# Kernel optimization log

Measured on AMD Instinct MI355X. Metric: run time of the kernel, lower is better.

Reference implementation:

```python
import jax, jax.numpy as jnp
import numpy as np

B, T, D, F0, F1 = 128, 256, 512, 2048, 1024
EPS = 1e-5  # BatchNorm1d eps


def _bn_relu(x, gamma, beta):
    # training-mode BatchNorm1d over the flattened (B*T) batch axis, then ReLU
    mu = x.mean(axis=0)
    var = x.var(axis=0)  # biased variance, as torch BN uses for normalization
    return jax.nn.relu((x - mu) * jax.lax.rsqrt(var + EPS) * gamma + beta)


def _lstm_cell(x, h, c, w_ih, w_hh, b):
    # torch LSTMCell gate order: i, f, g, o
    gates = x @ w_ih.T + h @ w_hh.T + b
    i, f, g, o = jnp.split(gates, 4, axis=-1)
    c = jax.nn.sigmoid(f) * c + jax.nn.sigmoid(i) * jnp.tanh(g)
    h = jax.nn.sigmoid(o) * jnp.tanh(c)
    return h, c


def setup_inputs() -> dict:
    key = jax.random.key(0)
    ks = jax.random.split(key, 24)
    s = 0.02
    inp = {
        "feat0": jax.random.normal(ks[0], (B, T, F0), jnp.float32),
        "feat1": jax.random.normal(ks[1], (B, T, F1), jnp.float32),
        "feat_mask": jnp.ones((B, T), jnp.float32),
        # visual embeddings (Linear + BN affine)
        "w_emb0": jax.random.normal(ks[2], (D, F0), jnp.float32) * s,
        "b_emb0": jnp.zeros((D,), jnp.float32),
        "gamma0": jnp.ones((D,), jnp.float32),
        "beta0": jnp.zeros((D,), jnp.float32),
        "w_emb1": jax.random.normal(ks[3], (D, F1), jnp.float32) * s,
        "b_emb1": jnp.zeros((D,), jnp.float32),
        "gamma1": jnp.ones((D,), jnp.float32),
        "beta1": jnp.zeros((D,), jnp.float32),
        # LSTMCell rgb
        "w_ih0": jax.random.normal(ks[4], (4 * D, D), jnp.float32) * s,
        "w_hh0": jax.random.normal(ks[5], (4 * D, D), jnp.float32) * s,
        "b_ih0": jnp.zeros((4 * D,), jnp.float32),
        "b_hh0": jnp.zeros((4 * D,), jnp.float32),
        # LSTMCell opfl
        "w_ih1": jax.random.normal(ks[6], (4 * D, D), jnp.float32) * s,
        "w_hh1": jax.random.normal(ks[7], (4 * D, D), jnp.float32) * s,
        "b_ih1": jnp.zeros((4 * D,), jnp.float32),
        "b_hh1": jnp.zeros((4 * D,), jnp.float32),
        # Gates: sigmoid(Linear(source)) * target
        "wg0": jax.random.normal(ks[8], (D, D), jnp.float32) * s,
        "bg0": jnp.zeros((D,), jnp.float32),
        "wg1": jax.random.normal(ks[9], (D, D), jnp.float32) * s,
        "bg1": jnp.zeros((D,), jnp.float32),
        # Fusion: tanh(W1 f1 + W2 f2 + b)
        "wf1": jax.random.normal(ks[10], (D, D), jnp.float32) * s,
        "wf2": jax.random.normal(ks[11], (D, D), jnp.float32) * s,
        "bf": jnp.zeros((D,), jnp.float32),
    }
    return inp


def reference(feat0, feat1, feat_mask,
              w_emb0, b_emb0, gamma0, beta0,
              w_emb1, b_emb1, gamma1, beta1,
              w_ih0, w_hh0, b_ih0, b_hh0,
              w_ih1, w_hh1, b_ih1, b_hh1,
              wg0, bg0, wg1, bg1,
              wf1, wf2, bf):
    Bv, Tv = feat0.shape[0], feat0.shape[1]
    # embed + BN(train mode) + ReLU (dropout = identity in eval)
    e0 = _bn_relu(feat0.reshape(-1, feat0.shape[-1]) @ w_emb0.T + b_emb0,
                  gamma0, beta0).reshape(Bv, Tv, -1)
    e1 = _bn_relu(feat1.reshape(-1, feat1.shape[-1]) @ w_emb1.T + b_emb1,
                  gamma1, beta1).reshape(Bv, Tv, -1)

    bc0 = b_ih0 + b_hh0
    bc1 = b_ih1 + b_hh1

    def step(carry, xs):
        h0, c0, h1, c1 = carry
        x0, x1, m = xs  # x: [B, D], m: [B]
        h0, c0 = _lstm_cell(x0, h0, c0, w_ih0, w_hh0, bc0)
        h1, c1 = _lstm_cell(x1, h1, c1, w_ih1, w_hh1, bc1)
        m = m[:, None]
        h0, c0, h1, c1 = h0 * m, c0 * m, h1 * m, c1 * m
        gate0 = jax.nn.sigmoid(h1 @ wg0.T + bg0) * h0  # gate_rgb(h1 -> h0)
        gate1 = jax.nn.sigmoid(h0 @ wg1.T + bg1) * h1  # gate_opfl(h0 -> h1)
        return (h0, c0, h1, c1), (gate0, gate1)

    z = jnp.zeros((Bv, w_hh0.shape[-1]), e0.dtype)
    xs = (e0.transpose(1, 0, 2), e1.transpose(1, 0, 2), feat_mask.T)
    _, (o0, o1) = jax.lax.scan(step, (z, z, z, z), xs)  # [T, B, D]
    o0 = o0.transpose(1, 0, 2)
    o1 = o1.transpose(1, 0, 2)
    # Fusion: tanh(W1 o0 + W2 o1 + b)
    return jnp.tanh(jnp.einsum('btd,ed->bte', o0, wf1)
                    + jnp.einsum('btd,ed->bte', o1, wf2) + bf)
```

## Files before the change

kernel.cpp:

```cpp
#include <hip/hip_runtime.h>
#include <math.h>


typedef short s16x8 __attribute__((ext_vector_type(8)));
typedef float f32x4 __attribute__((ext_vector_type(4)));
typedef float f32x16 __attribute__((ext_vector_type(16)));
typedef unsigned short u16;

__device__ __forceinline__ float sigmoidf_(float x){ return 1.0f/(1.0f+expf(-x)); }

__device__ __forceinline__ u16 f2bf(float x){
  unsigned int u = __float_as_uint(x);
  unsigned int r = u + 0x7fffu + ((u>>16)&1u);
  return (u16)(r>>16);
}
__device__ __forceinline__ float bf2f(u16 s){ return __uint_as_float(((unsigned int)s)<<16); }

__global__ __launch_bounds__(256) void split_plain(const float* __restrict__ src,
                                                   u16* __restrict__ hi, u16* __restrict__ lo, int n)
{
  int i = blockIdx.x*256 + threadIdx.x;
  if (i < n){
    float v = src[i];
    u16 h = f2bf(v);
    hi[i] = h;
    lo[i] = f2bf(v - bf2f(h));
  }
}

__global__ __launch_bounds__(256) void split_fragW(const float* __restrict__ src,
                                                   u16* __restrict__ hi, u16* __restrict__ lo,
                                                   int N, int K)
{
  int i = blockIdx.x*256 + threadIdx.x;
  if (i >= N*K) return;
  int n = i / K, k = i - n*K;
  float v = src[i];
  u16 h = f2bf(v), l2 = f2bf(v - bf2f(h));
  size_t off = ((((size_t)(k>>4)*(N/32) + (n>>5))*64) + ((k>>3)&1)*32 + (n&31))*8 + (k&7);
  hi[off] = h; lo[off] = l2;
}

__global__ __launch_bounds__(256) void split_gates2(const float* __restrict__ wih,
                                                    const float* __restrict__ whh,
                                                    const float* __restrict__ bih,
                                                    const float* __restrict__ bhh,
                                                    u16* __restrict__ hi, u16* __restrict__ lo,
                                                    float* __restrict__ bc)
{
  int np = blockIdx.x;
  int d = np>>2, q = np&3;
  int orow = q*512 + d;
  for (int k = threadIdx.x; k < 1024; k += 256){
    float v = (k < 512) ? wih[(size_t)orow*512 + k] : whh[(size_t)orow*512 + (k-512)];
    u16 h = f2bf(v), l2 = f2bf(v - bf2f(h));
    size_t off = (((size_t)(k>>4)*64 + (np>>5))*64 + ((k>>3)&1)*32 + (np&31))*8 + (k&7);
    hi[off] = h; lo[off] = l2;
  }
  if (threadIdx.x == 0) bc[np] = bih[orow] + bhh[orow];
}

__global__ __launch_bounds__(256) void gemm_emb(
    const float* __restrict__ A, const u16* __restrict__ Whi, const u16* __restrict__ Wlo,
    const float* __restrict__ bias, float* __restrict__ out, int K)
{
  __shared__ u16 Ah[128][40];
  __shared__ u16 Al[128][40];
  __shared__ u16 Wh[128][40];
  __shared__ u16 Wl[128][40];

  int bx = blockIdx.x;
  int nt = bx & 3, mt = bx >> 2;
  int m0 = mt*128, n0 = nt*128;
  int tid = threadIdx.x, lane = tid & 63, w = tid >> 6;
  int wm = (w>>1)*64, wn = (w&1)*64;

  f32x4 acc[4][4];
  #pragma unroll
  for (int i=0;i<4;i++)
    #pragma unroll
    for (int j=0;j<4;j++) acc[i][j] = (f32x4){0.f,0.f,0.f,0.f};

  for (int k0=0; k0<K; k0+=32){
    #pragma unroll
    for (int p=0;p<4;p++){
      int fi = p*256 + tid;
      int r = fi>>3, c = fi&7;
      float4 v = *(const float4*)&A[(size_t)(m0+r)*K + k0 + c*4];
      u16 h0=f2bf(v.x), h1=f2bf(v.y), h2=f2bf(v.z), h3=f2bf(v.w);
      u16 l0=f2bf(v.x-bf2f(h0)), l1=f2bf(v.y-bf2f(h1)), l2=f2bf(v.z-bf2f(h2)), l3=f2bf(v.w-bf2f(h3));
      uint2 ph = { (unsigned)h0 | ((unsigned)h1<<16), (unsigned)h2 | ((unsigned)h3<<16) };
      uint2 pl = { (unsigned)l0 | ((unsigned)l1<<16), (unsigned)l2 | ((unsigned)l3<<16) };
      *(uint2*)&Ah[r][c*4] = ph;
      *(uint2*)&Al[r][c*4] = pl;
    }
    #pragma unroll
    for (int p=0;p<2;p++){
      int fi = p*256 + tid;
      int r = fi>>2, c = fi&3;
      uint4 vh = *(const uint4*)&Whi[(size_t)(n0+r)*K + k0 + c*8];
      uint4 vl = *(const uint4*)&Wlo[(size_t)(n0+r)*K + k0 + c*8];
      *(uint4*)&Wh[r][c*8] = vh;
      *(uint4*)&Wl[r][c*8] = vl;
    }
    __syncthreads();
    s16x8 ah[4], al[4];
    #pragma unroll
    for (int mf=0;mf<4;mf++){
      ah[mf] = *(const s16x8*)&Ah[wm + mf*16 + (lane&15)][(lane>>4)*8];
      al[mf] = *(const s16x8*)&Al[wm + mf*16 + (lane&15)][(lane>>4)*8];
    }
    #pragma unroll
    for (int nf=0;nf<4;nf++){
      s16x8 wh = *(const s16x8*)&Wh[wn + nf*16 + (lane&15)][(lane>>4)*8];
      s16x8 wl = *(const s16x8*)&Wl[wn + nf*16 + (lane&15)][(lane>>4)*8];
      #pragma unroll
      for (int mf=0;mf<4;mf++){
        acc[mf][nf] = __builtin_amdgcn_mfma_f32_16x16x32_bf16(ah[mf], wh, acc[mf][nf], 0,0,0);
        acc[mf][nf] = __builtin_amdgcn_mfma_f32_16x16x32_bf16(ah[mf], wl, acc[mf][nf], 0,0,0);
        acc[mf][nf] = __builtin_amdgcn_mfma_f32_16x16x32_bf16(al[mf], wh, acc[mf][nf], 0,0,0);
      }
    }
    __syncthreads();
  }
  #pragma unroll
  for (int mf=0;mf<4;mf++){
    #pragma unroll
    for (int nf=0;nf<4;nf++){
      int col = n0 + wn + nf*16 + (lane&15);
      int row0 = m0 + wm + mf*16 + (lane>>4)*4;
      float b = bias[col];
      #pragma unroll
      for (int g=0; g<4; ++g){
        out[(size_t)(row0+g)*512 + col] = acc[mf][nf][g] + b;
      }
    }
  }
}

__global__ __launch_bounds__(256) void bn_stats1(const float* __restrict__ Y,
                                                 float* __restrict__ psum,
                                                 float* __restrict__ psq)
{
  int blk = blockIdx.x;
  int tid = threadIdx.x;
  const float* base = Y + (size_t)blk*256*512;
  float sx=0.f, sy=0.f, qx=0.f, qy=0.f;
  for (int r=0;r<256;r++){
    float2 v = *(const float2*)&base[(size_t)r*512 + tid*2];
    sx += v.x; sy += v.y; qx += v.x*v.x; qy += v.y*v.y;
  }
  psum[(size_t)blk*512 + tid*2]   = sx;
  psum[(size_t)blk*512 + tid*2+1] = sy;
  psq [(size_t)blk*512 + tid*2]   = qx;
  psq [(size_t)blk*512 + tid*2+1] = qy;
}

__global__ __launch_bounds__(512) void bn_stats2(const float* __restrict__ psum,
                                                 const float* __restrict__ psq,
                                                 float* __restrict__ mean,
                                                 float* __restrict__ scale)
{
  int c = threadIdx.x;
  float s=0.f, q=0.f;
  for (int b=0;b<128;b++){ s += psum[(size_t)b*512+c]; q += psq[(size_t)b*512+c]; }
  float mu = s * (1.0f/32768.0f);
  float var = q * (1.0f/32768.0f) - mu*mu;
  mean[c] = mu;
  scale[c] = rsqrtf(var + 1e-5f);
}

__global__ __launch_bounds__(256) void bn_apply_split(const float* __restrict__ Y,
                                                      const float* __restrict__ mean,
                                                      const float* __restrict__ scale,
                                                      const float* __restrict__ gamma,
                                                      const float* __restrict__ beta,
                                                      u16* __restrict__ ehi, u16* __restrict__ elo)
{
  size_t idx = (size_t)blockIdx.x*256 + threadIdx.x;
  int r = (int)(idx >> 6);
  int c0 = (int)(idx & 63) * 8;
  int b = r >> 8, t = r & 255;
  float4 v0 = *(const float4*)&Y[(size_t)r*512 + c0];
  float4 v1 = *(const float4*)&Y[(size_t)r*512 + c0 + 4];
  float vv[8] = {v0.x,v0.y,v0.z,v0.w,v1.x,v1.y,v1.z,v1.w};
  unsigned int hw[4], lw[4];
  #pragma unroll
  for (int u=0;u<8;u+=2){
    float xa = fmaxf((vv[u]  -mean[c0+u])  *scale[c0+u]  *gamma[c0+u]  +beta[c0+u],   0.f);
    float xb = fmaxf((vv[u+1]-mean[c0+u+1])*scale[c0+u+1]*gamma[c0+u+1]+beta[c0+u+1], 0.f);
    u16 ha = f2bf(xa), hb = f2bf(xb);
    u16 la = f2bf(xa - bf2f(ha)), lb = f2bf(xb - bf2f(hb));
    hw[u>>1] = (unsigned)ha | ((unsigned)hb<<16);
    lw[u>>1] = (unsigned)la | ((unsigned)lb<<16);
  }
  size_t off = (size_t)t*65536 + ((((size_t)(c0>>4)*4 + (b>>5))*64) + ((c0>>3)&1)*32 + (b&31))*8;
  uint4 ph = {hw[0],hw[1],hw[2],hw[3]};
  uint4 pl = {lw[0],lw[1],lw[2],lw[3]};
  *(uint4*)&ehi[off] = ph;
  *(uint4*)&elo[off] = pl;
}

__global__ __launch_bounds__(256) void zero_init(int* __restrict__ bar,
                                                 u16* __restrict__ H0hi, u16* __restrict__ H0lo,
                                                 u16* __restrict__ H1hi, u16* __restrict__ H1lo)
{
  int i = blockIdx.x*256 + threadIdx.x;
  if (i < 5120) bar[i] = 0;
  H0hi[i]=0; H0lo[i]=0; H1hi[i]=0; H1lo[i]=0;
}

struct ScanArgs {
  const u16 *e0hi, *e0lo, *e1hi, *e1lo;
  const u16 *wr0hi, *wr0lo, *wr1hi, *wr1lo;
  const float *bc0, *bc1, *mask;
  u16 *H0hi, *H0lo, *H1hi, *H1lo;
  int *flags;
  int *gen;
};

__global__ __launch_bounds__(256) void scan_all(ScanArgs A)
{
  __shared__ u16 Wlds[64][64][8];
  __shared__ float red[2][2][16][65];
  __shared__ int sig;
  __shared__ int fcnt;

  int bx = blockIdx.x;
  int ci = bx>>7, s = (bx>>1)&63, rh = bx&1;
  int cb = bx & 127;
  int tid = threadIdx.x, lane = tid&63, w = tid>>6;
  int khalf = w>>1, pr = w&1;
  int rt = rh*2 + pr;
  bool mast = (cb == 0);

  int* flags = A.flags + ci*128*16;
  int* gen   = A.gen   + ci*32*16;

  const u16* ehi = ci? A.e1hi : A.e0hi;
  const u16* elo = ci? A.e1lo : A.e0lo;
  const u16* whi = ci? A.wr1hi : A.wr0hi;
  const u16* wlo = ci? A.wr1lo : A.wr0lo;
  const float* bc = ci? A.bc1 : A.bc0;
  u16* Hhi = ci? A.H1hi : A.H0hi;
  u16* Hlo = ci? A.H1lo : A.H0lo;

  if (tid == 0){ sig = 0; fcnt = 0; }

  for (int it=0; it<16; ++it){
    int cid = it*256 + tid;
    int ks = cid>>6, l8 = cid&63;
    const u16* src = whi + (((size_t)ks*64 + s)*64 + l8)*8;
    *(uint4*)&Wlds[ks][l8][0] = *(const uint4*)src;
  }
  __syncthreads();

  int q = lane&3;
  int np = s*32 + (lane&31);
  int d  = np>>2;
  float bcv = bc[np];
  float creg[4] = {0.f,0.f,0.f,0.f};

  for (int t=0; t<256; ++t){
    size_t abase = (size_t)t*65536;

    if (khalf == 0){
      f32x16 a0=(f32x16)(0.f), a1=(f32x16)(0.f), a2=(f32x16)(0.f);
      #pragma unroll 4
      for (int kk=0; kk<32; ++kk){
        size_t aoff = abase + ((size_t)(kk*4 + rt)*64 + lane)*8;
        s16x8 fah = *(const s16x8*)(ehi + aoff);
        s16x8 fal = *(const s16x8*)(elo + aoff);
        s16x8 fwh = *(const s16x8*)&Wlds[kk][lane][0];
        s16x8 fwl = *(const s16x8*)(wlo + (((size_t)kk*64 + s)*64 + lane)*8);
        a0 = __builtin_amdgcn_mfma_f32_32x32x16_bf16(fah, fwh, a0, 0,0,0);
        a1 = __builtin_amdgcn_mfma_f32_32x32x16_bf16(fah, fwl, a1, 0,0,0);
        a2 = __builtin_amdgcn_mfma_f32_32x32x16_bf16(fal, fwh, a2, 0,0,0);
      }
      f32x16 t3 = a0 + a1 + a2;
      #pragma unroll
      for (int e=0;e<16;e++) red[t&1][pr][e][lane] = t3[e];
      __syncthreads();
    } else {
      if (lane == 0){
        while (__hip_atomic_load(&gen[(cb&31)*16], __ATOMIC_RELAXED, __HIP_MEMORY_SCOPE_AGENT) < t)
          __builtin_amdgcn_s_sleep(1);
      }
      asm volatile("" ::: "memory");

      f32x16 a0=(f32x16)(0.f), a1=(f32x16)(0.f), a2=(f32x16)(0.f);
      #pragma unroll 8
      for (int kk=0; kk<32; ++kk){
        size_t aoff = abase + ((size_t)(kk*4 + rt)*64 + lane)*8;
        s16x8 fah = *(const s16x8*)(Hhi + aoff);
        s16x8 fal = *(const s16x8*)(Hlo + aoff);
        int ks = 32 + kk;
        s16x8 fwh = *(const s16x8*)&Wlds[ks][lane][0];
        s16x8 fwl = *(const s16x8*)(wlo + (((size_t)ks*64 + s)*64 + lane)*8);
        a0 = __builtin_amdgcn_mfma_f32_32x32x16_bf16(fah, fwh, a0, 0,0,0);
        a1 = __builtin_amdgcn_mfma_f32_32x32x16_bf16(fah, fwl, a1, 0,0,0);
        a2 = __builtin_amdgcn_mfma_f32_32x32x16_bf16(fal, fwh, a2, 0,0,0);
      }
      f32x16 mine = a0 + a1 + a2;
      __syncthreads();

      f32x16 tot;
      #pragma unroll
      for (int e=0;e<16;e++) tot[e] = mine[e] + red[t&1][pr][e][lane];

      size_t hSlot = (size_t)(t+1)*65536;
      #pragma unroll
      for (int r=0;r<16;r++){
        float pre = tot[r] + bcv;
        float act = (q==2) ? tanhf(pre) : sigmoidf_(pre);
        float v1 = __shfl_xor(act, 1);
        float v2 = __shfl_xor(act, 2);
        float v3 = __shfl_xor(v1, 2);
        float gi = (q==0)? act : (q==1)? v1 : (q==2)? v2 : v3;
        float gf = (q==1)? act : (q==0)? v1 : (q==3)? v2 : v3;
        float gg = (q==2)? act : (q==3)? v1 : (q==0)? v2 : v3;
        float go = (q==3)? act : (q==2)? v1 : (q==1)? v2 : v3;
        if (q == (r&3)){
          int ri = r>>2;
          int row = rh*64 + pr*32 + (r&3) + 8*ri + 4*(lane>>5);
          float cold = creg[ri];
          float cn = gf*cold + gi*gg;
          float h  = go*tanhf(cn);
          float mv = A.mask[(size_t)row*256 + t];
          cn *= mv; h *= mv;
          creg[ri] = cn;
          u16 hh = f2bf(h), hl = f2bf(h - bf2f(hh));
          size_t hoff = hSlot + ((((size_t)(d>>4)*4 + (row>>5))*64) + ((d>>3)&1)*32 + (row&31))*8 + (d&7);
          __hip_atomic_store((short*)&Hhi[hoff], (short)hh, __ATOMIC_RELAXED, __HIP_MEMORY_SCOPE_AGENT);
          __hip_atomic_store((short*)&Hlo[hoff], (short)hl, __ATOMIC_RELAXED, __HIP_MEMORY_SCOPE_AGENT);
        }
      }
      asm volatile("s_waitcnt vmcnt(0)" ::: "memory");
      if (lane == 0) atomicAdd(&sig, 1);

      if (mast){
        int fi = tid - 128;
        if (fi >= 1){
          while (__hip_atomic_load(&flags[fi*16], __ATOMIC_RELAXED, __HIP_MEMORY_SCOPE_AGENT) < t+1)
            __builtin_amdgcn_s_sleep(1);
          atomicAdd(&fcnt, 1);
        }
        if (tid == 128){
          while (__hip_atomic_load(&sig, __ATOMIC_RELAXED, __HIP_MEMORY_SCOPE_WORKGROUP) < 2*(t+1))
            __builtin_amdgcn_s_sleep(1);
          while (__hip_atomic_load(&fcnt, __ATOMIC_RELAXED, __HIP_MEMORY_SCOPE_WORKGROUP) < 127*(t+1))
            __builtin_amdgcn_s_sleep(1);
        }
        if (w == 2 && lane < 32){
          __hip_atomic_store(&gen[lane*16], t+1, __ATOMIC_RELAXED, __HIP_MEMORY_SCOPE_AGENT);
        }
      } else {
        if (tid == 128){
          while (__hip_atomic_load(&sig, __ATOMIC_RELAXED, __HIP_MEMORY_SCOPE_WORKGROUP) < 2*(t+1))
            __builtin_amdgcn_s_sleep(1);
          __hip_atomic_store(&flags[cb*16], t+1, __ATOMIC_RELAXED, __HIP_MEMORY_SCOPE_AGENT);
        }
      }
    }
  }
}

template<int MODE>
__global__ __launch_bounds__(256,1) void gemm_fr(
    const u16* __restrict__ Ahi,  const u16* __restrict__ Alo,
    const u16* __restrict__ A2hi, const u16* __restrict__ A2lo,
    const u16* __restrict__ Whi,  const u16* __restrict__ Wlo,
    const u16* __restrict__ W2hi, const u16* __restrict__ W2lo,
    const float* __restrict__ bias,
    const u16* __restrict__ OtHi, const u16* __restrict__ OtLo,
    u16* __restrict__ outHi, u16* __restrict__ outLo,
    float* __restrict__ outF)
{
  int bx = blockIdx.x;
  int nt = bx & 7, mt = bx >> 3;
  int n0 = nt*64;
  int tid = threadIdx.x, lane = tid & 63, w = tid >> 6;
  size_t aBase = (size_t)mt*65536;

  f32x16 a0[2], a1[2], a2[2];
  #pragma unroll
  for (int c=0;c<2;c++){
    a0[c]=(f32x16)(0.f); a1[c]=(f32x16)(0.f); a2[c]=(f32x16)(0.f);
  }

  const int npair = (MODE==1) ? 2 : 1;
  for (int pair=0; pair<npair; ++pair){
    const u16* ah = pair ? A2hi : Ahi;
    const u16* al = pair ? A2lo : Alo;
    const u16* wh = pair ? W2hi : Whi;
    const u16* wl = pair ? W2lo : Wlo;
    #pragma unroll 2
    for (int kk=0; kk<32; ++kk){
      size_t aoff = aBase + (((size_t)kk*4 + w)*64 + lane)*8;
      s16x8 fah = *(const s16x8*)(ah + aoff);
      s16x8 fal = *(const s16x8*)(al + aoff);
      #pragma unroll
      for (int c=0;c<2;c++){
        size_t woff = (((size_t)kk*16 + nt*2 + c)*64 + lane)*8;
        s16x8 fwh = *(const s16x8*)(wh + woff);
        s16x8 fwl = *(const s16x8*)(wl + woff);
        a0[c] = __builtin_amdgcn_mfma_f32_32x32x16_bf16(fah, fwh, a0[c], 0,0,0);
        a1[c] = __builtin_amdgcn_mfma_f32_32x32x16_bf16(fah, fwl, a1[c], 0,0,0);
        a2[c] = __builtin_amdgcn_mfma_f32_32x32x16_bf16(fal, fwh, a2[c], 0,0,0);
      }
    }
  }

  #pragma unroll
  for (int c=0;c<2;c++){
    f32x16 acc = a0[c] + a1[c] + a2[c];
    int col = n0 + c*32 + (lane&31);
    float b = bias[col];
    #pragma unroll
    for (int r=0;r<16;r++){
      int row = w*32 + (r&3) + 8*(r>>2) + 4*(lane>>5);
      float v = acc[r] + b;
      if (MODE==0){
        size_t foff = aBase + ((((size_t)(col>>4)*4 + w)*64) + ((col>>3)&1)*32 + (row&31))*8 + (col&7);
        float other = bf2f(OtHi[foff]) + bf2f(OtLo[foff]);
        v = sigmoidf_(v) * other;
        u16 hh = f2bf(v);
        u16 hl = f2bf(v - bf2f(hh));
        outHi[foff] = hh;
        outLo[foff] = hl;
      } else {
        v = tanhf(v);
        outF[((size_t)row*256 + mt)*512 + col] = v;
      }
    }
  }
}

extern "C" void kernel_launch(void* const* d_in, const int* in_sizes, int n_in,
                              void* d_out, int out_size, void* d_ws, size_t ws_size,
                              hipStream_t stream)
{
  const float* feat0  = (const float*)d_in[0];
  const float* feat1  = (const float*)d_in[1];
  const float* fmask  = (const float*)d_in[2];
  const float* w_emb0 = (const float*)d_in[3];
  const float* b_emb0 = (const float*)d_in[4];
  const float* gamma0 = (const float*)d_in[5];
  const float* beta0  = (const float*)d_in[6];
  const float* w_emb1 = (const float*)d_in[7];
  const float* b_emb1 = (const float*)d_in[8];
  const float* gamma1 = (const float*)d_in[9];
  const float* beta1  = (const float*)d_in[10];
  const float* w_ih0  = (const float*)d_in[11];
  const float* w_hh0  = (const float*)d_in[12];
  const float* b_ih0  = (const float*)d_in[13];
  const float* b_hh0  = (const float*)d_in[14];
  const float* w_ih1  = (const float*)d_in[15];
  const float* w_hh1  = (const float*)d_in[16];
  const float* b_ih1  = (const float*)d_in[17];
  const float* b_hh1  = (const float*)d_in[18];
  const float* wg0    = (const float*)d_in[19];
  const float* bg0    = (const float*)d_in[20];
  const float* wg1    = (const float*)d_in[21];
  const float* bg1    = (const float*)d_in[22];
  const float* wf1    = (const float*)d_in[23];
  const float* wf2    = (const float*)d_in[24];
  const float* bf     = (const float*)d_in[25];
  float* out = (float*)d_out;

  char* ws = (char*)d_ws;
  u16* e0hi = (u16*)(ws + 0);
  u16* e0lo = (u16*)(ws + 33554432);
  u16* e1hi = (u16*)(ws + 67108864);
  u16* e1lo = (u16*)(ws + 100663296);
  u16* H0hi = (u16*)(ws + 134217728);
  u16* H0lo = (u16*)(ws + 167903232);
  u16* H1hi = (u16*)(ws + 201588736);
  u16* H1lo = (u16*)(ws + 235274240);
  int*   barp  = (int*)(ws + 269484032);
  float* psum  = (float*)(ws + 269484032);
  float* psq   = (float*)(ws + 269746176);
  float* meanb = (float*)(ws + 270008320);
  float* scaleb= (float*)(ws + 270010368);
  float* bc0   = (float*)(ws + 270012416);
  float* bc1   = (float*)(ws + 270020608);
  u16* wr0hi = (u16*)(ws + 270028800);
  u16* wr0lo = (u16*)(ws + 274223104);
  u16* wr1hi = (u16*)(ws + 278417408);
  u16* wr1lo = (u16*)(ws + 282611712);
  u16* we0hi = (u16*)(ws + 286806016);
  u16* we0lo = (u16*)(ws + 288903168);
  u16* we1hi = (u16*)(ws + 291000320);
  u16* we1lo = (u16*)(ws + 292048896);
  u16* wg0hi = (u16*)(ws + 293097472);
  u16* wg0lo = (u16*)(ws + 293621760);
  u16* wg1hi = (u16*)(ws + 294146048);
  u16* wg1lo = (u16*)(ws + 294670336);
  u16* wf1hi = (u16*)(ws + 295194624);
  u16* wf1lo = (u16*)(ws + 295718912);
  u16* wf2hi = (u16*)(ws + 296243200);
  u16* wf2lo = (u16*)(ws + 296767488);
  float* Ytmp = (float*)(ws + 134217728);

  split_gates2<<<dim3(2048), dim3(256), 0, stream>>>(w_ih0, w_hh0, b_ih0, b_hh0, wr0hi, wr0lo, bc0);
  split_gates2<<<dim3(2048), dim3(256), 0, stream>>>(w_ih1, w_hh1, b_ih1, b_hh1, wr1hi, wr1lo, bc1);
  split_plain<<<dim3(4096), dim3(256), 0, stream>>>(w_emb0, we0hi, we0lo, 1048576);
  split_plain<<<dim3(2048), dim3(256), 0, stream>>>(w_emb1, we1hi, we1lo, 524288);
  split_fragW<<<dim3(1024), dim3(256), 0, stream>>>(wg0, wg0hi, wg0lo, 512, 512);
  split_fragW<<<dim3(1024), dim3(256), 0, stream>>>(wg1, wg1hi, wg1lo, 512, 512);
  split_fragW<<<dim3(1024), dim3(256), 0, stream>>>(wf1, wf1hi, wf1lo, 512, 512);
  split_fragW<<<dim3(1024), dim3(256), 0, stream>>>(wf2, wf2hi, wf2lo, 512, 512);

  gemm_emb<<<dim3(1024), dim3(256), 0, stream>>>(feat0, we0hi, we0lo, b_emb0, Ytmp, 2048);
  bn_stats1<<<dim3(128), dim3(256), 0, stream>>>(Ytmp, psum, psq);
  bn_stats2<<<dim3(1),   dim3(512), 0, stream>>>(psum, psq, meanb, scaleb);
  bn_apply_split<<<dim3(8192), dim3(256), 0, stream>>>(Ytmp, meanb, scaleb, gamma0, beta0, e0hi, e0lo);

  gemm_emb<<<dim3(1024), dim3(256), 0, stream>>>(feat1, we1hi, we1lo, b_emb1, Ytmp, 1024);
  bn_stats1<<<dim3(128), dim3(256), 0, stream>>>(Ytmp, psum, psq);
  bn_stats2<<<dim3(1),   dim3(512), 0, stream>>>(psum, psq, meanb, scaleb);
  bn_apply_split<<<dim3(8192), dim3(256), 0, stream>>>(Ytmp, meanb, scaleb, gamma1, beta1, e1hi, e1lo);

  zero_init<<<dim3(256), dim3(256), 0, stream>>>(barp, H0hi, H0lo, H1hi, H1lo);
  ScanArgs sa;
  sa.e0hi=e0hi; sa.e0lo=e0lo; sa.e1hi=e1hi; sa.e1lo=e1lo;
  sa.wr0hi=wr0hi; sa.wr0lo=wr0lo; sa.wr1hi=wr1hi; sa.wr1lo=wr1lo;
  sa.bc0=bc0; sa.bc1=bc1; sa.mask=fmask;
  sa.H0hi=H0hi; sa.H0lo=H0lo; sa.H1hi=H1hi; sa.H1lo=H1lo;
  sa.flags=barp; sa.gen=barp + 128*16*2;
  scan_all<<<dim3(256), dim3(256), 0, stream>>>(sa);

  gemm_fr<0><<<dim3(2048), dim3(256), 0, stream>>>(
      H1hi + 65536, H1lo + 65536, nullptr, nullptr,
      wg0hi, wg0lo, nullptr, nullptr, bg0,
      H0hi + 65536, H0lo + 65536, e0hi, e0lo, nullptr);
  gemm_fr<0><<<dim3(2048), dim3(256), 0, stream>>>(
      H0hi + 65536, H0lo + 65536, nullptr, nullptr,
      wg1hi, wg1lo, nullptr, nullptr, bg1,
      H1hi + 65536, H1lo + 65536, e1hi, e1lo, nullptr);
  gemm_fr<1><<<dim3(2048), dim3(256), 0, stream>>>(
      e0hi, e0lo, e1hi, e1lo,
      wf1hi, wf1lo, wf2hi, wf2lo, bf,
      nullptr, nullptr, nullptr, nullptr, out);
}
```

Measured before the change: 7.582 ms.

## Halve scan blocks and replace master-gather barrier with all-to-all flag polling

The persistent LSTM scan kernel now runs 128 blocks instead of 256, each computing two 32-column gate tiles, so the number of blocks joining each per-timestep grid barrier is halved. The two-level barrier (a master block gathers all flags and then broadcasts a generation counter) is replaced by each wave's 64 lanes polling all 64 peer flags directly, which removes one hop of cross-block latency per step. Only the recurrent (h) half of the high weight tiles is cached in LDS now, while the input-projection weights are read from global memory. In exchange, each block does twice the MFMA work per step and issues more global loads.

```diff
diff --git a/kernel.cpp b/kernel.cpp
--- a/kernel.cpp
+++ b/kernel.cpp
@@ -206,7 +206,7 @@
                                                  u16* __restrict__ H1hi, u16* __restrict__ H1lo)
 {
   int i = blockIdx.x*256 + threadIdx.x;
-  if (i < 5120) bar[i] = 0;
+  if (i < 2048) bar[i] = 0;
   H0hi[i]=0; H0lo[i]=0; H1hi[i]=0; H1lo[i]=0;
 }
 
@@ -216,26 +216,22 @@
   const float *bc0, *bc1, *mask;
   u16 *H0hi, *H0lo, *H1hi, *H1lo;
   int *flags;
-  int *gen;
 };
 
 __global__ __launch_bounds__(256) void scan_all(ScanArgs A)
 {
-  __shared__ u16 Wlds[64][64][8];
-  __shared__ float red[2][2][16][65];
+  __shared__ u16 Wlds[32][2][64][8];
+  __shared__ float red[2][2][2][16][64];
   __shared__ int sig;
-  __shared__ int fcnt;
 
   int bx = blockIdx.x;
-  int ci = bx>>7, s = (bx>>1)&63, rh = bx&1;
-  int cb = bx & 127;
+  int ci = bx>>6, s = (bx>>1)&31, rh = bx&1;
+  int cb = bx & 63;
   int tid = threadIdx.x, lane = tid&63, w = tid>>6;
   int khalf = w>>1, pr = w&1;
   int rt = rh*2 + pr;
-  bool mast = (cb == 0);
-
-  int* flags = A.flags + ci*128*16;
-  int* gen   = A.gen   + ci*32*16;
+
+  int* flags = A.flags + ci*64*16;
 
   const u16* ehi = ci? A.e1hi : A.e0hi;
   const u16* elo = ci? A.e1lo : A.e0lo;
@@ -245,121 +241,126 @@
   u16* Hhi = ci? A.H1hi : A.H0hi;
   u16* Hlo = ci? A.H1lo : A.H0lo;
 
-  if (tid == 0){ sig = 0; fcnt = 0; }
+  if (tid == 0) sig = 0;
 
   for (int it=0; it<16; ++it){
     int cid = it*256 + tid;
-    int ks = cid>>6, l8 = cid&63;
-    const u16* src = whi + (((size_t)ks*64 + s)*64 + l8)*8;
-    *(uint4*)&Wlds[ks][l8][0] = *(const uint4*)src;
+    int ks = cid>>7, ct = (cid>>6)&1, l8 = cid&63;
+    const u16* src = whi + ((((size_t)(ks+32)*64) + (s*2+ct))*64 + l8)*8;
+    *(uint4*)&Wlds[ks][ct][l8][0] = *(const uint4*)src;
   }
   __syncthreads();
 
   int q = lane&3;
-  int np = s*32 + (lane&31);
-  int d  = np>>2;
-  float bcv = bc[np];
-  float creg[4] = {0.f,0.f,0.f,0.f};
+  float bcv[2];
+  bcv[0] = bc[s*64 + (lane&31)];
+  bcv[1] = bc[s*64 + 32 + (lane&31)];
+  float creg[2][4];
+  #pragma unroll
+  for (int c=0;c<2;c++)
+    #pragma unroll
+    for (int i=0;i<4;i++) creg[c][i]=0.f;
 
   for (int t=0; t<256; ++t){
     size_t abase = (size_t)t*65536;
 
     if (khalf == 0){
-      f32x16 a0=(f32x16)(0.f), a1=(f32x16)(0.f), a2=(f32x16)(0.f);
-      #pragma unroll 4
+      f32x16 a0[2], a1[2], a2[2];
+      #pragma unroll
+      for (int c=0;c<2;c++){ a0[c]=(f32x16)(0.f); a1[c]=(f32x16)(0.f); a2[c]=(f32x16)(0.f); }
+      #pragma unroll 2
       for (int kk=0; kk<32; ++kk){
         size_t aoff = abase + ((size_t)(kk*4 + rt)*64 + lane)*8;
         s16x8 fah = *(const s16x8*)(ehi + aoff);
         s16x8 fal = *(const s16x8*)(elo + aoff);
-        s16x8 fwh = *(const s16x8*)&Wlds[kk][lane][0];
-        s16x8 fwl = *(const s16x8*)(wlo + (((size_t)kk*64 + s)*64 + lane)*8);
-        a0 = __builtin_amdgcn_mfma_f32_32x32x16_bf16(fah, fwh, a0, 0,0,0);
-        a1 = __builtin_amdgcn_mfma_f32_32x32x16_bf16(fah, fwl, a1, 0,0,0);
-        a2 = __builtin_amdgcn_mfma_f32_32x32x16_bf16(fal, fwh, a2, 0,0,0);
-      }
-      f32x16 t3 = a0 + a1 + a2;
-      #pragma unroll
-      for (int e=0;e<16;e++) red[t&1][pr][e][lane] = t3[e];
+        #pragma unroll
+        for (int c=0;c<2;c++){
+          size_t woff = (((size_t)kk*64 + (s*2+c))*64 + lane)*8;
+          s16x8 fwh = *(const s16x8*)(whi + woff);
+          s16x8 fwl = *(const s16x8*)(wlo + woff);
+          a0[c] = __builtin_amdgcn_mfma_f32_32x32x16_bf16(fah, fwh, a0[c], 0,0,0);
+          a1[c] = __builtin_amdgcn_mfma_f32_32x32x16_bf16(fah, fwl, a1[c], 0,0,0);
+          a2[c] = __builtin_amdgcn_mfma_f32_32x32x16_bf16(fal, fwh, a2[c], 0,0,0);
+        }
+      }
+      #pragma unroll
+      for (int c=0;c<2;c++){
+        f32x16 t3 = a0[c] + a1[c] + a2[c];
+        #pragma unroll
+        for (int e=0;e<16;e++) red[t&1][pr][c][e][lane] = t3[e];
+      }
       __syncthreads();
     } else {
-      if (lane == 0){
-        while (__hip_atomic_load(&gen[(cb&31)*16], __ATOMIC_RELAXED, __HIP_MEMORY_SCOPE_AGENT) < t)
-          __builtin_amdgcn_s_sleep(1);
+      {
+        int v;
+        do {
+          v = __hip_atomic_load(&flags[lane*16], __ATOMIC_RELAXED, __HIP_MEMORY_SCOPE_AGENT);
+          if (v < t) __builtin_amdgcn_s_sleep(1);
+        } while (v < t);
       }
       asm volatile("" ::: "memory");
 
-      f32x16 a0=(f32x16)(0.f), a1=(f32x16)(0.f), a2=(f32x16)(0.f);
-      #pragma unroll 8
+      f32x16 a0[2], a1[2], a2[2];
+      #pragma unroll
+      for (int c=0;c<2;c++){ a0[c]=(f32x16)(0.f); a1[c]=(f32x16)(0.f); a2[c]=(f32x16)(0.f); }
+      #pragma unroll 4
       for (int kk=0; kk<32; ++kk){
         size_t aoff = abase + ((size_t)(kk*4 + rt)*64 + lane)*8;
         s16x8 fah = *(const s16x8*)(Hhi + aoff);
         s16x8 fal = *(const s16x8*)(Hlo + aoff);
-        int ks = 32 + kk;
-        s16x8 fwh = *(const s16x8*)&Wlds[ks][lane][0];
-        s16x8 fwl = *(const s16x8*)(wlo + (((size_t)ks*64 + s)*64 + lane)*8);
-        a0 = __builtin_amdgcn_mfma_f32_32x32x16_bf16(fah, fwh, a0, 0,0,0);
-        a1 = __builtin_amdgcn_mfma_f32_32x32x16_bf16(fah, fwl, a1, 0,0,0);
-        a2 = __builtin_amdgcn_mfma_f32_32x32x16_bf16(fal, fwh, a2, 0,0,0);
-      }
-      f32x16 mine = a0 + a1 + a2;
+        #pragma unroll
+        for (int c=0;c<2;c++){
+          s16x8 fwh = *(const s16x8*)&Wlds[kk][c][lane][0];
+          s16x8 fwl = *(const s16x8*)(wlo + ((((size_t)(kk+32)*64) + (s*2+c))*64 + lane)*8);
+          a0[c] = __builtin_amdgcn_mfma_f32_32x32x16_bf16(fah, fwh, a0[c], 0,0,0);
+          a1[c] = __builtin_amdgcn_mfma_f32_32x32x16_bf16(fah, fwl, a1[c], 0,0,0);
+          a2[c] = __builtin_amdgcn_mfma_f32_32x32x16_bf16(fal, fwh, a2[c], 0,0,0);
+        }
+      }
       __syncthreads();
 
-      f32x16 tot;
-      #pragma unroll
-      for (int e=0;e<16;e++) tot[e] = mine[e] + red[t&1][pr][e][lane];
-
       size_t hSlot = (size_t)(t+1)*65536;
       #pragma unroll
-      for (int r=0;r<16;r++){
-        float pre = tot[r] + bcv;
-        float act = (q==2) ? tanhf(pre) : sigmoidf_(pre);
-        float v1 = __shfl_xor(act, 1);
-        float v2 = __shfl_xor(act, 2);
-        float v3 = __shfl_xor(v1, 2);
-        float gi = (q==0)? act : (q==1)? v1 : (q==2)? v2 : v3;
-        float gf = (q==1)? act : (q==0)? v1 : (q==3)? v2 : v3;
-        float gg = (q==2)? act : (q==3)? v1 : (q==0)? v2 : v3;
-        float go = (q==3)? act : (q==2)? v1 : (q==1)? v2 : v3;
-        if (q == (r&3)){
-          int ri = r>>2;
-          int row = rh*64 + pr*32 + (r&3) + 8*ri + 4*(lane>>5);
-          float cold = creg[ri];
-          float cn = gf*cold + gi*gg;
-          float h  = go*tanhf(cn);
-          float mv = A.mask[(size_t)row*256 + t];
-          cn *= mv; h *= mv;
-          creg[ri] = cn;
-          u16 hh = f2bf(h), hl = f2bf(h - bf2f(hh));
-          size_t hoff = hSlot + ((((size_t)(d>>4)*4 + (row>>5))*64) + ((d>>3)&1)*32 + (row&31))*8 + (d&7);
-          __hip_atomic_store((short*)&Hhi[hoff], (short)hh, __ATOMIC_RELAXED, __HIP_MEMORY_SCOPE_AGENT);
-          __hip_atomic_store((short*)&Hlo[hoff], (short)hl, __ATOMIC_RELAXED, __HIP_MEMORY_SCOPE_AGENT);
+      for (int c=0;c<2;c++){
+        f32x16 tot = a0[c] + a1[c] + a2[c];
+        #pragma unroll
+        for (int e=0;e<16;e++) tot[e] += red[t&1][pr][c][e][lane];
+        int col_l = c*32 + (lane&31);
+        int d = (s*64 + col_l) >> 2;
+        float bcvc = bcv[c];
+        #pragma unroll
+        for (int r=0;r<16;r++){
+          float pre = tot[r] + bcvc;
+          float act = (q==2) ? tanhf(pre) : sigmoidf_(pre);
+          float v1 = __shfl_xor(act, 1);
+          float v2 = __shfl_xor(act, 2);
+          float v3 = __shfl_xor(v1, 2);
+          float gi = (q==0)? act : (q==1)? v1 : (q==2)? v2 : v3;
+          float gf = (q==1)? act : (q==0)? v1 : (q==3)? v2 : v3;
+          float gg = (q==2)? act : (q==3)? v1 : (q==0)? v2 : v3;
+          float go = (q==3)? act : (q==2)? v1 : (q==1)? v2 : v3;
+          if (q == (r&3)){
+            int ri = r>>2;
+            int row = rh*64 + pr*32 + (r&3) + 8*ri + 4*(lane>>5);
+            float cold = creg[c][ri];
+            float cn = gf*cold + gi*gg;
+            float h  = go*tanhf(cn);
+            float mv = A.mask[(size_t)row*256 + t];
+            cn *= mv; h *= mv;
+            creg[c][ri] = cn;
+            u16 hh = f2bf(h), hl = f2bf(h - bf2f(hh));
+            size_t hoff = hSlot + ((((size_t)(d>>4)*4 + (row>>5))*64) + ((d>>3)&1)*32 + (row&31))*8 + (d&7);
+            __hip_atomic_store((short*)&Hhi[hoff], (short)hh, __ATOMIC_RELAXED, __HIP_MEMORY_SCOPE_AGENT);
+            __hip_atomic_store((short*)&Hlo[hoff], (short)hl, __ATOMIC_RELAXED, __HIP_MEMORY_SCOPE_AGENT);
+          }
         }
       }
       asm volatile("s_waitcnt vmcnt(0)" ::: "memory");
       if (lane == 0) atomicAdd(&sig, 1);
-
-      if (mast){
-        int fi = tid - 128;
-        if (fi >= 1){
-          while (__hip_atomic_load(&flags[fi*16], __ATOMIC_RELAXED, __HIP_MEMORY_SCOPE_AGENT) < t+1)
-            __builtin_amdgcn_s_sleep(1);
-          atomicAdd(&fcnt, 1);
-        }
-        if (tid == 128){
-          while (__hip_atomic_load(&sig, __ATOMIC_RELAXED, __HIP_MEMORY_SCOPE_WORKGROUP) < 2*(t+1))
-            __builtin_amdgcn_s_sleep(1);
-          while (__hip_atomic_load(&fcnt, __ATOMIC_RELAXED, __HIP_MEMORY_SCOPE_WORKGROUP) < 127*(t+1))
-            __builtin_amdgcn_s_sleep(1);
-        }
-        if (w == 2 && lane < 32){
-          __hip_atomic_store(&gen[lane*16], t+1, __ATOMIC_RELAXED, __HIP_MEMORY_SCOPE_AGENT);
-        }
-      } else {
-        if (tid == 128){
-          while (__hip_atomic_load(&sig, __ATOMIC_RELAXED, __HIP_MEMORY_SCOPE_WORKGROUP) < 2*(t+1))
-            __builtin_amdgcn_s_sleep(1);
-          __hip_atomic_store(&flags[cb*16], t+1, __ATOMIC_RELAXED, __HIP_MEMORY_SCOPE_AGENT);
-        }
+      if (tid == 128){
+        while (__hip_atomic_load(&sig, __ATOMIC_RELAXED, __HIP_MEMORY_SCOPE_WORKGROUP) < 2*(t+1))
+          __builtin_amdgcn_s_sleep(1);
+        __hip_atomic_store(&flags[cb*16], t+1, __ATOMIC_RELAXED, __HIP_MEMORY_SCOPE_AGENT);
       }
     }
   }
@@ -527,8 +528,8 @@
   sa.wr0hi=wr0hi; sa.wr0lo=wr0lo; sa.wr1hi=wr1hi; sa.wr1lo=wr1lo;
   sa.bc0=bc0; sa.bc1=bc1; sa.mask=fmask;
   sa.H0hi=H0hi; sa.H0lo=H0lo; sa.H1hi=H1hi; sa.H1lo=H1lo;
-  sa.flags=barp; sa.gen=barp + 128*16*2;
-  scan_all<<<dim3(256), dim3(256), 0, stream>>>(sa);
+  sa.flags=barp;
+  scan_all<<<dim3(128), dim3(256), 0, stream>>>(sa);
 
   gemm_fr<0><<<dim3(2048), dim3(256), 0, stream>>>(
       H1hi + 65536, H1lo + 65536, nullptr, nullptr,
```

New measurement: 10.07 ms. +32.8%, slower.

## Replace master-gathered grid barrier with direct flag polling and cache recurrent lo weights in LDS

Applied to the files above, without the earlier changes.

The per-step cross-block barrier in the persistent LSTM scan is changed from a two-hop scheme to a one-hop scheme. Before, a master block gathered 127 flags and then broadcast a generation counter. Now each block's recurrent-half wave polls all 128 per-block flags directly, using one lane per pair of flags. The change also stages the low bf16 part of the recurrent weights in LDS instead of reading it from global memory on each step. The aim is to cut barrier latency on the serial 256-step critical path and remove global loads from the recurrent matmul. The cost is more polling traffic on the flag lines and extra LDS use per block, which could limit occupancy.

```diff
diff --git a/kernel.cpp b/kernel.cpp
--- a/kernel.cpp
+++ b/kernel.cpp
@@ -206,7 +206,7 @@
                                                  u16* __restrict__ H1hi, u16* __restrict__ H1lo)
 {
   int i = blockIdx.x*256 + threadIdx.x;
-  if (i < 5120) bar[i] = 0;
+  if (i < 4096) bar[i] = 0;
   H0hi[i]=0; H0lo[i]=0; H1hi[i]=0; H1lo[i]=0;
 }
 
@@ -216,15 +216,14 @@
   const float *bc0, *bc1, *mask;
   u16 *H0hi, *H0lo, *H1hi, *H1lo;
   int *flags;
-  int *gen;
 };
 
 __global__ __launch_bounds__(256) void scan_all(ScanArgs A)
 {
-  __shared__ u16 Wlds[64][64][8];
+  __shared__ u16 WldsHi[64][64][8];
+  __shared__ u16 WldsLo[32][64][8];
   __shared__ float red[2][2][16][65];
   __shared__ int sig;
-  __shared__ int fcnt;
 
   int bx = blockIdx.x;
   int ci = bx>>7, s = (bx>>1)&63, rh = bx&1;
@@ -232,10 +231,8 @@
   int tid = threadIdx.x, lane = tid&63, w = tid>>6;
   int khalf = w>>1, pr = w&1;
   int rt = rh*2 + pr;
-  bool mast = (cb == 0);
 
   int* flags = A.flags + ci*128*16;
-  int* gen   = A.gen   + ci*32*16;
 
   const u16* ehi = ci? A.e1hi : A.e0hi;
   const u16* elo = ci? A.e1lo : A.e0lo;
@@ -245,13 +242,19 @@
   u16* Hhi = ci? A.H1hi : A.H0hi;
   u16* Hlo = ci? A.H1lo : A.H0lo;
 
-  if (tid == 0){ sig = 0; fcnt = 0; }
+  if (tid == 0) sig = 0;
 
   for (int it=0; it<16; ++it){
     int cid = it*256 + tid;
     int ks = cid>>6, l8 = cid&63;
     const u16* src = whi + (((size_t)ks*64 + s)*64 + l8)*8;
-    *(uint4*)&Wlds[ks][l8][0] = *(const uint4*)src;
+    *(uint4*)&WldsHi[ks][l8][0] = *(const uint4*)src;
+  }
+  for (int it=0; it<8; ++it){
+    int cid = it*256 + tid;
+    int ks = cid>>6, l8 = cid&63;
+    const u16* src = wlo + (((size_t)(ks+32)*64 + s)*64 + l8)*8;
+    *(uint4*)&WldsLo[ks][l8][0] = *(const uint4*)src;
   }
   __syncthreads();
 
@@ -271,7 +274,7 @@
         size_t aoff = abase + ((size_t)(kk*4 + rt)*64 + lane)*8;
         s16x8 fah = *(const s16x8*)(ehi + aoff);
         s16x8 fal = *(const s16x8*)(elo + aoff);
-        s16x8 fwh = *(const s16x8*)&Wlds[kk][lane][0];
+        s16x8 fwh = *(const s16x8*)&WldsHi[kk][lane][0];
         s16x8 fwl = *(const s16x8*)(wlo + (((size_t)kk*64 + s)*64 + lane)*8);
         a0 = __builtin_amdgcn_mfma_f32_32x32x16_bf16(fah, fwh, a0, 0,0,0);
         a1 = __builtin_amdgcn_mfma_f32_32x32x16_bf16(fah, fwl, a1, 0,0,0);
@@ -282,9 +285,13 @@
       for (int e=0;e<16;e++) red[t&1][pr][e][lane] = t3[e];
       __syncthreads();
     } else {
-      if (lane == 0){
-        while (__hip_atomic_load(&gen[(cb&31)*16], __ATOMIC_RELAXED, __HIP_MEMORY_SCOPE_AGENT) < t)
-          __builtin_amdgcn_s_sleep(1);
+      {
+        int v0, v1;
+        do {
+          v0 = __hip_atomic_load(&flags[lane*16],      __ATOMIC_RELAXED, __HIP_MEMORY_SCOPE_AGENT);
+          v1 = __hip_atomic_load(&flags[(lane+64)*16], __ATOMIC_RELAXED, __HIP_MEMORY_SCOPE_AGENT);
+          if (v0 < t || v1 < t) __builtin_amdgcn_s_sleep(1);
+        } while (v0 < t || v1 < t);
       }
       asm volatile("" ::: "memory");
 
@@ -294,9 +301,8 @@
         size_t aoff = abase + ((size_t)(kk*4 + rt)*64 + lane)*8;
         s16x8 fah = *(const s16x8*)(Hhi + aoff);
         s16x8 fal = *(const s16x8*)(Hlo + aoff);
-        int ks = 32 + kk;
-        s16x8 fwh = *(const s16x8*)&Wlds[ks][lane][0];
-        s16x8 fwl = *(const s16x8*)(wlo + (((size_t)ks*64 + s)*64 + lane)*8);
+        s16x8 fwh = *(const s16x8*)&WldsHi[32+kk][lane][0];
+        s16x8 fwl = *(const s16x8*)&WldsLo[kk][lane][0];
         a0 = __builtin_amdgcn_mfma_f32_32x32x16_bf16(fah, fwh, a0, 0,0,0);
         a1 = __builtin_amdgcn_mfma_f32_32x32x16_bf16(fah, fwl, a1, 0,0,0);
         a2 = __builtin_amdgcn_mfma_f32_32x32x16_bf16(fal, fwh, a2, 0,0,0);
@@ -337,29 +343,10 @@
       }
       asm volatile("s_waitcnt vmcnt(0)" ::: "memory");
       if (lane == 0) atomicAdd(&sig, 1);
-
-      if (mast){
-        int fi = tid - 128;
-        if (fi >= 1){
-          while (__hip_atomic_load(&flags[fi*16], __ATOMIC_RELAXED, __HIP_MEMORY_SCOPE_AGENT) < t+1)
-            __builtin_amdgcn_s_sleep(1);
-          atomicAdd(&fcnt, 1);
-        }
-        if (tid == 128){
-          while (__hip_atomic_load(&sig, __ATOMIC_RELAXED, __HIP_MEMORY_SCOPE_WORKGROUP) < 2*(t+1))
-            __builtin_amdgcn_s_sleep(1);
-          while (__hip_atomic_load(&fcnt, __ATOMIC_RELAXED, __HIP_MEMORY_SCOPE_WORKGROUP) < 127*(t+1))
-            __builtin_amdgcn_s_sleep(1);
-        }
-        if (w == 2 && lane < 32){
-          __hip_atomic_store(&gen[lane*16], t+1, __ATOMIC_RELAXED, __HIP_MEMORY_SCOPE_AGENT);
-        }
-      } else {
-        if (tid == 128){
-          while (__hip_atomic_load(&sig, __ATOMIC_RELAXED, __HIP_MEMORY_SCOPE_WORKGROUP) < 2*(t+1))
-            __builtin_amdgcn_s_sleep(1);
-          __hip_atomic_store(&flags[cb*16], t+1, __ATOMIC_RELAXED, __HIP_MEMORY_SCOPE_AGENT);
-        }
+      if (tid == 128){
+        while (__hip_atomic_load(&sig, __ATOMIC_RELAXED, __HIP_MEMORY_SCOPE_WORKGROUP) < 2*(t+1))
+          __builtin_amdgcn_s_sleep(1);
+        __hip_atomic_store(&flags[cb*16], t+1, __ATOMIC_RELAXED, __HIP_MEMORY_SCOPE_AGENT);
       }
     }
   }
@@ -527,7 +514,7 @@
   sa.wr0hi=wr0hi; sa.wr0lo=wr0lo; sa.wr1hi=wr1hi; sa.wr1lo=wr1lo;
   sa.bc0=bc0; sa.bc1=bc1; sa.mask=fmask;
   sa.H0hi=H0hi; sa.H0lo=H0lo; sa.H1hi=H1hi; sa.H1lo=H1lo;
-  sa.flags=barp; sa.gen=barp + 128*16*2;
+  sa.flags=barp;
   scan_all<<<dim3(256), dim3(256), 0, stream>>>(sa);
 
   gemm_fr<0><<<dim3(2048), dim3(256), 0, stream>>>(
```

After: 9.004 ms. +18.8%, slower.
